# Performance work log

Hardware: AMD Instinct MI355X
Metric: run time of the kernel (lower is better)

Reference implementation:

```python
import jax, jax.numpy as jnp
import numpy as np

E, D, A, F, K = 512, 1024, 128, 32, 31  # encoder_dim, decoder_dim, attention_dim, location_filters, kernel
B, T = 128, 512


def setup_inputs() -> dict:
    key = jax.random.key(0)
    ks = jax.random.split(key, 9)
    s = lambda *sh: 1.0 / np.sqrt(sh[-1])
    return {
        "encoder_outputs": jax.random.normal(ks[0], (B, T, E), jnp.float32),
        "decoder_state": jax.random.normal(ks[1], (B, D), jnp.float32),
        "prev_attention_weights": jax.random.uniform(ks[2], (B, T), jnp.float32),
        # parameters (torch Linear stores [out, in]; Conv1d [out, in, K])
        "W_enc": jax.random.normal(ks[3], (A, E), jnp.float32) * s(A, E),
        "W_dec": jax.random.normal(ks[4], (A, D), jnp.float32) * s(A, D),
        "conv_w": jax.random.normal(ks[5], (F, 1, K), jnp.float32) * (1.0 / np.sqrt(K)),
        "W_loc": jax.random.normal(ks[6], (A, F), jnp.float32) * s(A, F),
        "W_e": jax.random.normal(ks[7], (1, A), jnp.float32) * s(1, A),
        "b_e": jax.random.normal(ks[8], (1,), jnp.float32) * 0.01,
    }


def reference(encoder_outputs, decoder_state, prev_attention_weights,
              W_enc, W_dec, conv_w, W_loc, W_e, b_e):
    # encoder projection: [B,T,E] @ [E,A] -> [B,T,A]
    enc_p = jnp.einsum('bte,ae->bta', encoder_outputs, W_enc)
    # decoder projection: [B,D] -> [B,1,A]
    dec_p = jnp.einsum('bd,ad->ba', decoder_state, W_dec)[:, None, :]
    # location conv: [B,1,T] * [F,1,K] -> [B,F,T], 'same' padding
    loc = jax.lax.conv_general_dilated(
        prev_attention_weights[:, None, :], conv_w,
        window_strides=(1,), padding=[((K - 1) // 2, (K - 1) // 2)],
        dimension_numbers=('NCH', 'OIH', 'NCH'))
    # [B,F,T] -> [B,T,A]
    loc_p = jnp.einsum('bft,af->bta', loc, W_loc)
    # energies: [B,T]
    energies = jnp.einsum('bta,a->bt', jnp.tanh(enc_p + dec_p + loc_p), W_e[0]) + b_e[0]
    attention_weights = jax.nn.softmax(energies, axis=1)
    # context: [B,T] x [B,T,E] -> [B,E]
    context_vector = jnp.einsum('bt,bte->be', attention_weights, encoder_outputs)
    return context_vector, attention_weights
```

## Files before the change

kernel.cpp:

```cpp
#include <hip/hip_runtime.h>
#include <hip/hip_bf16.h>
#include <math.h>

namespace {
constexpr int EDIM  = 512;
constexpr int DDIM  = 1024;
constexpr int ADIM  = 128;
constexpr int FDIM  = 32;
constexpr int KW    = 31;
constexpr int BATCH = 128;
constexpr int TDIM  = 512;

constexpr int LSTR = 40;
constexpr int TILE = 128 * LSTR;

typedef __attribute__((ext_vector_type(8))) short short8;
typedef __attribute__((ext_vector_type(4))) float floatx4;

__device__ __forceinline__ float fast_tanh(float x) {
  x = fminf(9.0f, fmaxf(-9.0f, x));
  float e = __expf(2.0f * x);
  return (e - 1.0f) / (e + 1.0f);
}

__device__ __forceinline__ ushort2 pack_bf16(float x, float y) {
  union { __hip_bfloat162 h; ushort2 u; } cv;
  cv.h = __float22bfloat162_rn(make_float2(x, y));
  return cv.u;
}

__device__ __forceinline__ short8 pack8(floatx4 a, floatx4 b) {
  union { ushort2 u[4]; short8 v; } o;
  o.u[0] = pack_bf16(a[0], a[1]); o.u[1] = pack_bf16(a[2], a[3]);
  o.u[2] = pack_bf16(b[0], b[1]); o.u[3] = pack_bf16(b[2], b[3]);
  return o.v;
}

__device__ __forceinline__ int ld_acq(int* p) {
  return __hip_atomic_load(p, __ATOMIC_ACQUIRE, __HIP_MEMORY_SCOPE_WORKGROUP);
}
__device__ __forceinline__ void add_rel(int* p) {
  __hip_atomic_fetch_add(p, 1, __ATOMIC_RELEASE, __HIP_MEMORY_SCOPE_WORKGROUP);
}

__global__ __launch_bounds__(256)
void dec_proj_kernel(const float* __restrict__ dec,
                     const float* __restrict__ Wdec,
                     float* __restrict__ dec_p) {
  int b = blockIdx.x, az = blockIdx.y;
  int tid = threadIdx.x;
  int al = tid >> 3, seg = tid & 7;
  int a = az * 32 + al;
  const float* dv = dec + (size_t)b * DDIM;
  const float* wv = Wdec + (size_t)a * DDIM;
  float s = 0.f;
  #pragma unroll 8
  for (int it = 0; it < 32; ++it) {
    int d = it * 32 + seg * 4;
    float4 d4 = *(const float4*)(dv + d);
    float4 w4 = *(const float4*)(wv + d);
    s += d4.x * w4.x + d4.y * w4.y + d4.z * w4.z + d4.w * w4.w;
  }
  s += __shfl_xor(s, 1, 64);
  s += __shfl_xor(s, 2, 64);
  s += __shfl_xor(s, 4, 64);
  if (seg == 0) dec_p[b * ADIM + a] = s;
}

__global__ __launch_bounds__(768)
void energies_kernel(const float* __restrict__ enc,
                     const float* __restrict__ Wenc,
                     const float* __restrict__ pa,
                     const float* __restrict__ convw,
                     const float* __restrict__ Wloc,
                     const float* __restrict__ We,
                     const float* __restrict__ be,
                     const float* __restrict__ dec_p,
                     float* __restrict__ energ) {
  __shared__ ushort tiles[2 * 2 * TILE];
  __shared__ ushort convS[4096];
  __shared__ float pa_s[160];
  __shared__ float cw_t[KW * 32];
  __shared__ int ready_a[2], ready_b[2], done_c[2], conv_done;

  const int tid  = threadIdx.x;
  const int b    = blockIdx.y;
  const int t0b  = blockIdx.x * 128;
  const int wave = tid >> 6, lane = tid & 63;

  if (tid == 0) {
    ready_a[0] = ready_a[1] = ready_b[0] = ready_b[1] = 0;
    done_c[0] = done_c[1] = 0;
    conv_done = 0;
  }
  if (tid >= 512 && tid < 512 + 158) {
    int gt = t0b - 15 + (tid - 512);
    pa_s[tid - 512] = (gt >= 0 && gt < TDIM) ? pa[b * TDIM + gt] : 0.f;
  }
  if (tid < 512)
    for (int id = tid; id < FDIM * KW; id += 512)
      cw_t[(id % KW) * 32 + (id / KW)] = convw[id];
  __syncthreads();

  if (wave >= 8) {
    const bool isA = (wave < 10);
    const int p = wave & 1;
    const float* gbase = isA ? enc + ((size_t)(b * TDIM + t0b)) * EDIM : Wenc;
    ushort* lbase = tiles + (isA ? 0 : TILE);
    int* myready = isA ? ready_a : ready_b;

    floatx4 v[8];
    #pragma unroll
    for (int j = 0; j < 4; ++j) {
      int idx = j * 64 + lane;
      int row = p * 64 + (idx >> 2), c = idx & 3;
      const float* g = gbase + (size_t)row * EDIM + c * 8;
      v[2 * j]     = *(const floatx4*)g;
      v[2 * j + 1] = *(const floatx4*)(g + 4);
    }

    for (int kt = 0; kt < 16; ++kt) {
      const int s = kt & 1, i = kt >> 1;
      if (kt >= 2)
        while (ld_acq(&done_c[s]) < 8 * i) __builtin_amdgcn_s_sleep(10);
      ushort* slot = lbase + s * 2 * TILE;
      #pragma unroll
      for (int j = 0; j < 4; ++j) {
        int idx = j * 64 + lane;
        int row = p * 64 + (idx >> 2), c = idx & 3;
        *(short8*)&slot[row * LSTR + c * 8] = pack8(v[2 * j], v[2 * j + 1]);
      }
      __threadfence_block();
      if (lane == 0) add_rel(&myready[s]);
      if (kt < 15) {
        #pragma unroll
        for (int j = 0; j < 4; ++j) {
          int idx = j * 64 + lane;
          int row = p * 64 + (idx >> 2), c = idx & 3;
          const float* g = gbase + (size_t)row * EDIM + (kt + 1) * 32 + c * 8;
          v[2 * j]     = *(const floatx4*)g;
          v[2 * j + 1] = *(const floatx4*)(g + 4);
        }
      }
    }
    return;
  }

  const int lc = lane & 15, lq = lane >> 4;

  {
    const int tl = tid >> 2, fg = tid & 3;
    float cv[8] = {0.f, 0.f, 0.f, 0.f, 0.f, 0.f, 0.f, 0.f};
    #pragma unroll
    for (int k = 0; k < KW; ++k) {
      float p = pa_s[tl + k];
      floatx4 c0 = *(const floatx4*)&cw_t[k * 32 + fg * 8];
      floatx4 c1 = *(const floatx4*)&cw_t[k * 32 + fg * 8 + 4];
      #pragma unroll
      for (int n = 0; n < 4; ++n) cv[n] += p * c0[n];
      #pragma unroll
      for (int n = 0; n < 4; ++n) cv[4 + n] += p * c1[n];
    }
    *(short8*)&convS[tl * 32 + fg * 8] =
        pack8((floatx4){cv[0], cv[1], cv[2], cv[3]},
              (floatx4){cv[4], cv[5], cv[6], cv[7]});
  }
  __threadfence_block();
  if (lane == 0) add_rel(&conv_done);

  floatx4 acc[8];
  #pragma unroll
  for (int aT = 0; aT < 8; ++aT) acc[aT] = (floatx4){0.f, 0.f, 0.f, 0.f};

  for (int kt = 0; kt < 16; ++kt) {
    const int s = kt & 1, i = kt >> 1;
    const int need = 2 * (i + 1);
    while (ld_acq(&ready_a[s]) < need || ld_acq(&ready_b[s]) < need)
      __builtin_amdgcn_s_sleep(6);
    const ushort* As_ = tiles + s * 2 * TILE;
    const ushort* Bs_ = As_ + TILE;
    short8 af = *(const short8*)&As_[(wave * 16 + lc) * LSTR + lq * 8];
    #pragma unroll
    for (int aT = 0; aT < 8; ++aT) {
      short8 bf = *(const short8*)&Bs_[(aT * 16 + lc) * LSTR + lq * 8];
      acc[aT] = __builtin_amdgcn_mfma_f32_16x16x32_bf16(af, bf, acc[aT], 0, 0, 0);
    }
    if (lane == 0) add_rel(&done_c[s]);
  }

  while (ld_acq(&conv_done) < 8) __builtin_amdgcn_s_sleep(6);
  {
    short8 afl = *(const short8*)&convS[(wave * 16 + lc) * 32 + lq * 8];
    #pragma unroll
    for (int aT = 0; aT < 8; ++aT) {
      const float* g = Wloc + (size_t)(aT * 16 + lc) * FDIM + lq * 8;
      short8 bfl = pack8(*(const floatx4*)g, *(const floatx4*)(g + 4));
      acc[aT] = __builtin_amdgcn_mfma_f32_16x16x32_bf16(afl, bfl, acc[aT], 0, 0, 0);
    }
  }

  const float be0 = be[0];
  float dpv[8], wev[8];
  #pragma unroll
  for (int aT = 0; aT < 8; ++aT) {
    int a = aT * 16 + lc;
    dpv[aT] = dec_p[b * ADIM + a];
    wev[aT] = We[a];
  }
  {
    float es[4] = {0.f, 0.f, 0.f, 0.f};
    #pragma unroll
    for (int aT = 0; aT < 8; ++aT)
      #pragma unroll
      for (int i = 0; i < 4; ++i)
        es[i] += fast_tanh(acc[aT][i] + dpv[aT]) * wev[aT];
    #pragma unroll
    for (int m = 1; m < 16; m <<= 1)
      #pragma unroll
      for (int i = 0; i < 4; ++i) es[i] += __shfl_xor(es[i], m, 64);
    if (lc == 0) {
      floatx4 ev = {es[0] + be0, es[1] + be0, es[2] + be0, es[3] + be0};
      *(floatx4*)&energ[(size_t)b * TDIM + t0b + wave * 16 + lq * 4] = ev;
    }
  }
}

__global__ __launch_bounds__(256)
void softmax_context_kernel(const float* __restrict__ enc,
                            const float* __restrict__ energ,
                            float* __restrict__ attn,
                            float* __restrict__ ctx) {
  __shared__ float aw[TDIM];
  __shared__ float redm[4];
  __shared__ float reds[4];
  __shared__ float red2[8][128];
  const int b = blockIdx.y, ex = blockIdx.x, tid = threadIdx.x;
  const float* row = energ + (size_t)b * TDIM;
  float x0 = row[tid], x1 = row[tid + 256];
  float m = fmaxf(x0, x1);
  #pragma unroll
  for (int off = 32; off; off >>= 1) m = fmaxf(m, __shfl_xor(m, off, 64));
  int wid = tid >> 6, lane = tid & 63;
  if (lane == 0) redm[wid] = m;
  __syncthreads();
  m = fmaxf(fmaxf(redm[0], redm[1]), fmaxf(redm[2], redm[3]));
  float e0 = __expf(x0 - m), e1 = __expf(x1 - m);
  float s = e0 + e1;
  #pragma unroll
  for (int off = 32; off; off >>= 1) s += __shfl_xor(s, off, 64);
  if (lane == 0) reds[wid] = s;
  __syncthreads();
  s = reds[0] + reds[1] + reds[2] + reds[3];
  float inv = 1.0f / s;
  float w0 = e0 * inv, w1 = e1 * inv;
  aw[tid] = w0; aw[tid + 256] = w1;
  if (ex == 0) {
    attn[(size_t)b * TDIM + tid] = w0;
    attn[(size_t)b * TDIM + tid + 256] = w1;
  }
  __syncthreads();
  const int c4 = (tid & 31) * 4;
  const int h  = tid >> 5;
  const float* ep = enc + (size_t)b * TDIM * EDIM + ex * 128 + c4;
  float4 acc = make_float4(0.f, 0.f, 0.f, 0.f);
  #pragma unroll 16
  for (int t = h; t < TDIM; t += 8) {
    float w = aw[t];
    float4 v = *(const float4*)(ep + (size_t)t * EDIM);
    acc.x += w * v.x; acc.y += w * v.y; acc.z += w * v.z; acc.w += w * v.w;
  }
  *(float4*)&red2[h][c4] = acc;
  __syncthreads();
  if (tid < 128) {
    float sum = 0.f;
    #pragma unroll
    for (int g = 0; g < 8; ++g) sum += red2[g][tid];
    ctx[(size_t)b * EDIM + ex * 128 + tid] = sum;
  }
}

__global__ __launch_bounds__(256)
void softmax_context_inplace_kernel(const float* __restrict__ enc,
                                    float* __restrict__ attn,
                                    float* __restrict__ ctx) {
  __shared__ float aw[TDIM];
  __shared__ float redm[4];
  __shared__ float reds[4];
  const int b = blockIdx.y, tid = threadIdx.x;
  float* row = attn + (size_t)b * TDIM;
  float x0 = row[tid], x1 = row[tid + 256];
  float m = fmaxf(x0, x1);
  #pragma unroll
  for (int off = 32; off; off >>= 1) m = fmaxf(m, __shfl_xor(m, off, 64));
  int wid = tid >> 6, lane = tid & 63;
  if (lane == 0) redm[wid] = m;
  __syncthreads();
  m = fmaxf(fmaxf(redm[0], redm[1]), fmaxf(redm[2], redm[3]));
  float e0 = __expf(x0 - m), e1 = __expf(x1 - m);
  float s = e0 + e1;
  #pragma unroll
  for (int off = 32; off; off >>= 1) s += __shfl_xor(s, off, 64);
  if (lane == 0) reds[wid] = s;
  __syncthreads();
  s = reds[0] + reds[1] + reds[2] + reds[3];
  float inv = 1.0f / s;
  float w0 = e0 * inv, w1 = e1 * inv;
  row[tid] = w0; row[tid + 256] = w1;
  aw[tid] = w0; aw[tid + 256] = w1;
  __syncthreads();
  const float* ep = enc + ((size_t)b * TDIM) * EDIM;
  float a0 = 0.f, a1 = 0.f;
  #pragma unroll 8
  for (int t = 0; t < TDIM; ++t) {
    float w = aw[t];
    a0 += w * ep[(size_t)t * EDIM + tid];
    a1 += w * ep[(size_t)t * EDIM + tid + 256];
  }
  ctx[(size_t)b * EDIM + tid] = a0;
  ctx[(size_t)b * EDIM + tid + 256] = a1;
}

}

extern "C" void kernel_launch(void* const* d_in, const int* in_sizes, int n_in,
                              void* d_out, int out_size, void* d_ws, size_t ws_size,
                              hipStream_t stream) {
  const float* enc   = (const float*)d_in[0];
  const float* dec   = (const float*)d_in[1];
  const float* pa    = (const float*)d_in[2];
  const float* Wenc  = (const float*)d_in[3];
  const float* Wdec  = (const float*)d_in[4];
  const float* convw = (const float*)d_in[5];
  const float* Wloc  = (const float*)d_in[6];
  const float* We    = (const float*)d_in[7];
  const float* be    = (const float*)d_in[8];

  float* ctx  = (float*)d_out;
  float* attn = (float*)d_out + BATCH * EDIM;

  float* dec_p = (float*)d_ws;
  float* energ = dec_p + BATCH * ADIM;

  const size_t need = (size_t)(BATCH * ADIM + BATCH * TDIM) * sizeof(float);

  dim3 g1(BATCH, 4);
  dec_proj_kernel<<<g1, 256, 0, stream>>>(dec, Wdec, dec_p);

  dim3 g2(TDIM / 128, BATCH);
  if (ws_size >= need) {
    energies_kernel<<<g2, 768, 0, stream>>>(enc, Wenc, pa, convw, Wloc, We, be,
                                            dec_p, energ);
    dim3 g3(4, BATCH);
    softmax_context_kernel<<<g3, 256, 0, stream>>>(enc, energ, attn, ctx);
  } else {
    energies_kernel<<<g2, 768, 0, stream>>>(enc, Wenc, pa, convw, Wloc, We, be,
                                            dec_p, attn);
    dim3 g3(1, BATCH);
    softmax_context_inplace_kernel<<<g3, 256, 0, stream>>>(enc, attn, ctx);
  }
}
```

Before: 243.4 us.

## Fuse softmax and context into energies kernel with split-softmax last-block reduction

Each energies block now computes a local max and sum over its 128 time steps, forms unnormalized weights, and accumulates a partial context from the encoder tile it just covered. It writes those partials to the workspace. The last block per batch, found through an atomic counter reset in dec_proj, rescales and combines them into the final attention weights and context. This removes the separate softmax/context launch and its second full pass over encoder_outputs from global memory. The cost is extra shared memory, atomics and a serialized tail in the last block of each batch.

```diff
diff --git a/kernel.cpp b/kernel.cpp
--- a/kernel.cpp
+++ b/kernel.cpp
@@ -46,9 +46,11 @@
 __global__ __launch_bounds__(256)
 void dec_proj_kernel(const float* __restrict__ dec,
                      const float* __restrict__ Wdec,
-                     float* __restrict__ dec_p) {
+                     float* __restrict__ dec_p,
+                     int* __restrict__ counters) {
   int b = blockIdx.x, az = blockIdx.y;
   int tid = threadIdx.x;
+  if (counters && az == 0 && tid == 0) counters[b] = 0;
   int al = tid >> 3, seg = tid & 7;
   int a = az * 32 + al;
   const float* dv = dec + (size_t)b * DDIM;
@@ -67,6 +69,7 @@
   if (seg == 0) dec_p[b * ADIM + a] = s;
 }
 
+template <int FUSED>
 __global__ __launch_bounds__(768)
 void energies_kernel(const float* __restrict__ enc,
                      const float* __restrict__ Wenc,
@@ -76,16 +79,29 @@
                      const float* __restrict__ We,
                      const float* __restrict__ be,
                      const float* __restrict__ dec_p,
-                     float* __restrict__ energ) {
+                     float* __restrict__ energ,
+                     float* __restrict__ pm,
+                     float* __restrict__ ps,
+                     float* __restrict__ pctx,
+                     int*   __restrict__ counters,
+                     float* __restrict__ attn,
+                     float* __restrict__ ctx) {
   __shared__ ushort tiles[2 * 2 * TILE];
   __shared__ ushort convS[4096];
   __shared__ float pa_s[160];
   __shared__ float cw_t[KW * 32];
   __shared__ int ready_a[2], ready_b[2], done_c[2], conv_done;
+  __shared__ float e_s[128];
+  __shared__ float aw_s[128];
+  __shared__ float ms[2];
+  __shared__ float red2[6][512];
+  __shared__ float pmx[4], psx[4];
+  __shared__ int lastflag;
 
   const int tid  = threadIdx.x;
   const int b    = blockIdx.y;
-  const int t0b  = blockIdx.x * 128;
+  const int chunk = blockIdx.x;
+  const int t0b  = chunk * 128;
   const int wave = tid >> 6, lane = tid & 63;
 
   if (tid == 0) {
@@ -143,139 +159,150 @@
         }
       }
     }
-    return;
-  }
-
-  const int lc = lane & 15, lq = lane >> 4;
+  } else {
+    const int lc = lane & 15, lq = lane >> 4;
+
+    {
+      const int tl = tid >> 2, fg = tid & 3;
+      float cv[8] = {0.f, 0.f, 0.f, 0.f, 0.f, 0.f, 0.f, 0.f};
+      #pragma unroll
+      for (int k = 0; k < KW; ++k) {
+        float p = pa_s[tl + k];
+        floatx4 c0 = *(const floatx4*)&cw_t[k * 32 + fg * 8];
+        floatx4 c1 = *(const floatx4*)&cw_t[k * 32 + fg * 8 + 4];
+        #pragma unroll
+        for (int n = 0; n < 4; ++n) cv[n] += p * c0[n];
+        #pragma unroll
+        for (int n = 0; n < 4; ++n) cv[4 + n] += p * c1[n];
+      }
+      *(short8*)&convS[tl * 32 + fg * 8] =
+          pack8((floatx4){cv[0], cv[1], cv[2], cv[3]},
+                (floatx4){cv[4], cv[5], cv[6], cv[7]});
+    }
+    __threadfence_block();
+    if (lane == 0) add_rel(&conv_done);
+
+    floatx4 acc[8];
+    #pragma unroll
+    for (int aT = 0; aT < 8; ++aT) acc[aT] = (floatx4){0.f, 0.f, 0.f, 0.f};
+
+    for (int kt = 0; kt < 16; ++kt) {
+      const int s = kt & 1, i = kt >> 1;
+      const int need = 2 * (i + 1);
+      while (ld_acq(&ready_a[s]) < need || ld_acq(&ready_b[s]) < need)
+        __builtin_amdgcn_s_sleep(6);
+      const ushort* As_ = tiles + s * 2 * TILE;
+      const ushort* Bs_ = As_ + TILE;
+      short8 af = *(const short8*)&As_[(wave * 16 + lc) * LSTR + lq * 8];
+      #pragma unroll
+      for (int aT = 0; aT < 8; ++aT) {
+        short8 bf = *(const short8*)&Bs_[(aT * 16 + lc) * LSTR + lq * 8];
+        acc[aT] = __builtin_amdgcn_mfma_f32_16x16x32_bf16(af, bf, acc[aT], 0, 0, 0);
+      }
+      if (lane == 0) add_rel(&done_c[s]);
+    }
+
+    while (ld_acq(&conv_done) < 8) __builtin_amdgcn_s_sleep(6);
+    {
+      short8 afl = *(const short8*)&convS[(wave * 16 + lc) * 32 + lq * 8];
+      #pragma unroll
+      for (int aT = 0; aT < 8; ++aT) {
+        const float* g = Wloc + (size_t)(aT * 16 + lc) * FDIM + lq * 8;
+        short8 bfl = pack8(*(const floatx4*)g, *(const floatx4*)(g + 4));
+        acc[aT] = __builtin_amdgcn_mfma_f32_16x16x32_bf16(afl, bfl, acc[aT], 0, 0, 0);
+      }
+    }
+
+    const float be0 = be[0];
+    float dpv[8], wev[8];
+    #pragma unroll
+    for (int aT = 0; aT < 8; ++aT) {
+      int a = aT * 16 + lc;
+      dpv[aT] = dec_p[b * ADIM + a];
+      wev[aT] = We[a];
+    }
+    {
+      float es[4] = {0.f, 0.f, 0.f, 0.f};
+      #pragma unroll
+      for (int aT = 0; aT < 8; ++aT)
+        #pragma unroll
+        for (int i = 0; i < 4; ++i)
+          es[i] += fast_tanh(acc[aT][i] + dpv[aT]) * wev[aT];
+      #pragma unroll
+      for (int m = 1; m < 16; m <<= 1)
+        #pragma unroll
+        for (int i = 0; i < 4; ++i) es[i] += __shfl_xor(es[i], m, 64);
+      if (lc == 0) {
+        floatx4 ev = {es[0] + be0, es[1] + be0, es[2] + be0, es[3] + be0};
+        *(floatx4*)&energ[(size_t)b * TDIM + t0b + wave * 16 + lq * 4] = ev;
+        if (FUSED) *(floatx4*)&e_s[wave * 16 + lq * 4] = ev;
+      }
+    }
+  }
+
+  if constexpr (!FUSED) return;
+
+  __syncthreads();
+
+  if (wave == 0) {
+    float x0 = e_s[lane], x1 = e_s[lane + 64];
+    float m = fmaxf(x0, x1);
+    #pragma unroll
+    for (int off = 1; off < 64; off <<= 1) m = fmaxf(m, __shfl_xor(m, off, 64));
+    float sum = __expf(x0 - m) + __expf(x1 - m);
+    #pragma unroll
+    for (int off = 1; off < 64; off <<= 1) sum += __shfl_xor(sum, off, 64);
+    if (lane == 0) {
+      ms[0] = m;
+      pm[b * 4 + chunk] = m;
+      ps[b * 4 + chunk] = sum;
+    }
+  }
+  __syncthreads();
+  const float mI = ms[0];
+  if (tid < 128) aw_s[tid] = __expf(e_s[tid] - mI);
+  __syncthreads();
 
   {
-    const int tl = tid >> 2, fg = tid & 3;
-    float cv[8] = {0.f, 0.f, 0.f, 0.f, 0.f, 0.f, 0.f, 0.f};
-    #pragma unroll
-    for (int k = 0; k < KW; ++k) {
-      float p = pa_s[tl + k];
-      floatx4 c0 = *(const floatx4*)&cw_t[k * 32 + fg * 8];
-      floatx4 c1 = *(const floatx4*)&cw_t[k * 32 + fg * 8 + 4];
-      #pragma unroll
-      for (int n = 0; n < 4; ++n) cv[n] += p * c0[n];
-      #pragma unroll
-      for (int n = 0; n < 4; ++n) cv[4 + n] += p * c1[n];
-    }
-    *(short8*)&convS[tl * 32 + fg * 8] =
-        pack8((floatx4){cv[0], cv[1], cv[2], cv[3]},
-              (floatx4){cv[4], cv[5], cv[6], cv[7]});
-  }
-  __threadfence_block();
-  if (lane == 0) add_rel(&conv_done);
-
-  floatx4 acc[8];
-  #pragma unroll
-  for (int aT = 0; aT < 8; ++aT) acc[aT] = (floatx4){0.f, 0.f, 0.f, 0.f};
-
-  for (int kt = 0; kt < 16; ++kt) {
-    const int s = kt & 1, i = kt >> 1;
-    const int need = 2 * (i + 1);
-    while (ld_acq(&ready_a[s]) < need || ld_acq(&ready_b[s]) < need)
-      __builtin_amdgcn_s_sleep(6);
-    const ushort* As_ = tiles + s * 2 * TILE;
-    const ushort* Bs_ = As_ + TILE;
-    short8 af = *(const short8*)&As_[(wave * 16 + lc) * LSTR + lq * 8];
-    #pragma unroll
-    for (int aT = 0; aT < 8; ++aT) {
-      short8 bf = *(const short8*)&Bs_[(aT * 16 + lc) * LSTR + lq * 8];
-      acc[aT] = __builtin_amdgcn_mfma_f32_16x16x32_bf16(af, bf, acc[aT], 0, 0, 0);
-    }
-    if (lane == 0) add_rel(&done_c[s]);
-  }
-
-  while (ld_acq(&conv_done) < 8) __builtin_amdgcn_s_sleep(6);
-  {
-    short8 afl = *(const short8*)&convS[(wave * 16 + lc) * 32 + lq * 8];
-    #pragma unroll
-    for (int aT = 0; aT < 8; ++aT) {
-      const float* g = Wloc + (size_t)(aT * 16 + lc) * FDIM + lq * 8;
-      short8 bfl = pack8(*(const floatx4*)g, *(const floatx4*)(g + 4));
-      acc[aT] = __builtin_amdgcn_mfma_f32_16x16x32_bf16(afl, bfl, acc[aT], 0, 0, 0);
-    }
-  }
-
-  const float be0 = be[0];
-  float dpv[8], wev[8];
-  #pragma unroll
-  for (int aT = 0; aT < 8; ++aT) {
-    int a = aT * 16 + lc;
-    dpv[aT] = dec_p[b * ADIM + a];
-    wev[aT] = We[a];
-  }
-  {
-    float es[4] = {0.f, 0.f, 0.f, 0.f};
-    #pragma unroll
-    for (int aT = 0; aT < 8; ++aT)
-      #pragma unroll
-      for (int i = 0; i < 4; ++i)
-        es[i] += fast_tanh(acc[aT][i] + dpv[aT]) * wev[aT];
-    #pragma unroll
-    for (int m = 1; m < 16; m <<= 1)
-      #pragma unroll
-      for (int i = 0; i < 4; ++i) es[i] += __shfl_xor(es[i], m, 64);
-    if (lc == 0) {
-      floatx4 ev = {es[0] + be0, es[1] + be0, es[2] + be0, es[3] + be0};
-      *(floatx4*)&energ[(size_t)b * TDIM + t0b + wave * 16 + lq * 4] = ev;
-    }
-  }
-}
-
-__global__ __launch_bounds__(256)
-void softmax_context_kernel(const float* __restrict__ enc,
-                            const float* __restrict__ energ,
-                            float* __restrict__ attn,
-                            float* __restrict__ ctx) {
-  __shared__ float aw[TDIM];
-  __shared__ float redm[4];
-  __shared__ float reds[4];
-  __shared__ float red2[8][128];
-  const int b = blockIdx.y, ex = blockIdx.x, tid = threadIdx.x;
-  const float* row = energ + (size_t)b * TDIM;
-  float x0 = row[tid], x1 = row[tid + 256];
-  float m = fmaxf(x0, x1);
-  #pragma unroll
-  for (int off = 32; off; off >>= 1) m = fmaxf(m, __shfl_xor(m, off, 64));
-  int wid = tid >> 6, lane = tid & 63;
-  if (lane == 0) redm[wid] = m;
-  __syncthreads();
-  m = fmaxf(fmaxf(redm[0], redm[1]), fmaxf(redm[2], redm[3]));
-  float e0 = __expf(x0 - m), e1 = __expf(x1 - m);
-  float s = e0 + e1;
-  #pragma unroll
-  for (int off = 32; off; off >>= 1) s += __shfl_xor(s, off, 64);
-  if (lane == 0) reds[wid] = s;
-  __syncthreads();
-  s = reds[0] + reds[1] + reds[2] + reds[3];
-  float inv = 1.0f / s;
-  float w0 = e0 * inv, w1 = e1 * inv;
-  aw[tid] = w0; aw[tid + 256] = w1;
-  if (ex == 0) {
-    attn[(size_t)b * TDIM + tid] = w0;
-    attn[(size_t)b * TDIM + tid + 256] = w1;
-  }
-  __syncthreads();
-  const int c4 = (tid & 31) * 4;
-  const int h  = tid >> 5;
-  const float* ep = enc + (size_t)b * TDIM * EDIM + ex * 128 + c4;
-  float4 acc = make_float4(0.f, 0.f, 0.f, 0.f);
-  #pragma unroll 16
-  for (int t = h; t < TDIM; t += 8) {
-    float w = aw[t];
-    float4 v = *(const float4*)(ep + (size_t)t * EDIM);
-    acc.x += w * v.x; acc.y += w * v.y; acc.z += w * v.z; acc.w += w * v.w;
-  }
-  *(float4*)&red2[h][c4] = acc;
-  __syncthreads();
-  if (tid < 128) {
-    float sum = 0.f;
-    #pragma unroll
-    for (int g = 0; g < 8; ++g) sum += red2[g][tid];
-    ctx[(size_t)b * EDIM + ex * 128 + tid] = sum;
+    const int tg = tid >> 7;
+    const int c4 = (tid & 127) * 4;
+    const float* ep = enc + ((size_t)(b * TDIM + t0b)) * EDIM + c4;
+    float4 acc = make_float4(0.f, 0.f, 0.f, 0.f);
+    for (int t = tg; t < 128; t += 6) {
+      float w = aw_s[t];
+      float4 v = *(const float4*)(ep + (size_t)t * EDIM);
+      acc.x += w * v.x; acc.y += w * v.y; acc.z += w * v.z; acc.w += w * v.w;
+    }
+    *(float4*)&red2[tg][c4] = acc;
+  }
+  __syncthreads();
+  if (tid < 512) {
+    float v = 0.f;
+    #pragma unroll
+    for (int g = 0; g < 6; ++g) v += red2[g][tid];
+    pctx[((size_t)(b * 4 + chunk)) * EDIM + tid] = v;
+  }
+  __threadfence();
+  __syncthreads();
+  if (tid == 0)
+    lastflag = __hip_atomic_fetch_add(&counters[b], 1, __ATOMIC_ACQ_REL,
+                                      __HIP_MEMORY_SCOPE_AGENT);
+  __syncthreads();
+  if (lastflag != 3) return;
+
+  if (tid < 4) { pmx[tid] = pm[b * 4 + tid]; psx[tid] = ps[b * 4 + tid]; }
+  __syncthreads();
+  const float M = fmaxf(fmaxf(pmx[0], pmx[1]), fmaxf(pmx[2], pmx[3]));
+  float r0 = __expf(pmx[0] - M), r1 = __expf(pmx[1] - M);
+  float r2 = __expf(pmx[2] - M), r3 = __expf(pmx[3] - M);
+  const float S = psx[0] * r0 + psx[1] * r1 + psx[2] * r2 + psx[3] * r3;
+  const float inv = 1.0f / S;
+  if (tid < 512) {
+    float e = energ[(size_t)b * TDIM + tid];
+    attn[(size_t)b * TDIM + tid] = __expf(e - M) * inv;
+    const float* pc = pctx + (size_t)b * 4 * EDIM + tid;
+    float c = pc[0] * r0 + pc[EDIM] * r1 + pc[2 * EDIM] * r2 + pc[3 * EDIM] * r3;
+    ctx[(size_t)b * EDIM + tid] = c * inv;
   }
 }
 
@@ -340,21 +367,28 @@
 
   float* dec_p = (float*)d_ws;
   float* energ = dec_p + BATCH * ADIM;
-
-  const size_t need = (size_t)(BATCH * ADIM + BATCH * TDIM) * sizeof(float);
-
-  dim3 g1(BATCH, 4);
-  dec_proj_kernel<<<g1, 256, 0, stream>>>(dec, Wdec, dec_p);
+  float* pm    = energ + BATCH * TDIM;
+  float* ps    = pm + BATCH * 4;
+  float* pctx  = ps + BATCH * 4;
+  int*   cnts  = (int*)(pctx + (size_t)BATCH * 4 * EDIM);
+
+  const size_t need =
+      ((size_t)BATCH * ADIM + BATCH * TDIM + BATCH * 8 +
+       (size_t)BATCH * 4 * EDIM) * sizeof(float) + BATCH * sizeof(int);
 
   dim3 g2(TDIM / 128, BATCH);
   if (ws_size >= need) {
-    energies_kernel<<<g2, 768, 0, stream>>>(enc, Wenc, pa, convw, Wloc, We, be,
-                                            dec_p, energ);
-    dim3 g3(4, BATCH);
-    softmax_context_kernel<<<g3, 256, 0, stream>>>(enc, energ, attn, ctx);
+    dim3 g1(BATCH, 4);
+    dec_proj_kernel<<<g1, 256, 0, stream>>>(dec, Wdec, dec_p, cnts);
+    energies_kernel<1><<<g2, 768, 0, stream>>>(enc, Wenc, pa, convw, Wloc, We,
+                                               be, dec_p, energ, pm, ps, pctx,
+                                               cnts, attn, ctx);
   } else {
-    energies_kernel<<<g2, 768, 0, stream>>>(enc, Wenc, pa, convw, Wloc, We, be,
-                                            dec_p, attn);
+    dim3 g1(BATCH, 4);
+    dec_proj_kernel<<<g1, 256, 0, stream>>>(dec, Wdec, dec_p, nullptr);
+    energies_kernel<0><<<g2, 768, 0, stream>>>(enc, Wenc, pa, convw, Wloc, We,
+                                               be, dec_p, attn, nullptr, nullptr,
+                                               nullptr, nullptr, nullptr, nullptr);
     dim3 g3(1, BATCH);
     softmax_context_inplace_kernel<<<g3, 256, 0, stream>>>(enc, attn, ctx);
   }
```

Measured after the change: 409.8 us. +68.3%, slower.

## Replace producer/consumer warp specialization with uniform double-buffered loads and barriers

Applied to the files above, without the earlier changes.

The energies kernel previously used four dedicated producer waves that loaded encoder and weight tiles into shared memory and signalled consumer waves through workgroup-scope atomic flags with sleep-polling. Now all eight waves load their own slice of the next K-tile into registers, compute MFMAs on the current buffer, then store the next tile, with one __syncthreads per iteration. The conv result reuses the A buffer after the loop instead of its own array. This removes spin-wait polling and the extra waves, and cuts shared memory, at the cost of losing dedicated producer overlap and adding block-wide barriers.

```diff
diff --git a/kernel.cpp b/kernel.cpp
--- a/kernel.cpp
+++ b/kernel.cpp
@@ -12,7 +12,6 @@
 constexpr int TDIM  = 512;
 
 constexpr int LSTR = 40;
-constexpr int TILE = 128 * LSTR;
 
 typedef __attribute__((ext_vector_type(8))) short short8;
 typedef __attribute__((ext_vector_type(4))) float floatx4;
@@ -34,13 +33,6 @@
   o.u[0] = pack_bf16(a[0], a[1]); o.u[1] = pack_bf16(a[2], a[3]);
   o.u[2] = pack_bf16(b[0], b[1]); o.u[3] = pack_bf16(b[2], b[3]);
   return o.v;
-}
-
-__device__ __forceinline__ int ld_acq(int* p) {
-  return __hip_atomic_load(p, __ATOMIC_ACQUIRE, __HIP_MEMORY_SCOPE_WORKGROUP);
-}
-__device__ __forceinline__ void add_rel(int* p) {
-  __hip_atomic_fetch_add(p, 1, __ATOMIC_RELEASE, __HIP_MEMORY_SCOPE_WORKGROUP);
 }
 
 __global__ __launch_bounds__(256)
@@ -67,7 +59,7 @@
   if (seg == 0) dec_p[b * ADIM + a] = s;
 }
 
-__global__ __launch_bounds__(768)
+__global__ __launch_bounds__(512)
 void energies_kernel(const float* __restrict__ enc,
                      const float* __restrict__ Wenc,
                      const float* __restrict__ pa,
@@ -77,80 +69,37 @@
                      const float* __restrict__ be,
                      const float* __restrict__ dec_p,
                      float* __restrict__ energ) {
-  __shared__ ushort tiles[2 * 2 * TILE];
-  __shared__ ushort convS[4096];
+  __shared__ ushort A_s[2][128 * LSTR];
+  __shared__ ushort B_s[2][128 * LSTR];
+  __shared__ float cw_t[KW * 32];
   __shared__ float pa_s[160];
-  __shared__ float cw_t[KW * 32];
-  __shared__ int ready_a[2], ready_b[2], done_c[2], conv_done;
 
   const int tid  = threadIdx.x;
   const int b    = blockIdx.y;
   const int t0b  = blockIdx.x * 128;
   const int wave = tid >> 6, lane = tid & 63;
-
-  if (tid == 0) {
-    ready_a[0] = ready_a[1] = ready_b[0] = ready_b[1] = 0;
-    done_c[0] = done_c[1] = 0;
-    conv_done = 0;
-  }
-  if (tid >= 512 && tid < 512 + 158) {
-    int gt = t0b - 15 + (tid - 512);
-    pa_s[tid - 512] = (gt >= 0 && gt < TDIM) ? pa[b * TDIM + gt] : 0.f;
-  }
-  if (tid < 512)
-    for (int id = tid; id < FDIM * KW; id += 512)
-      cw_t[(id % KW) * 32 + (id / KW)] = convw[id];
-  __syncthreads();
-
-  if (wave >= 8) {
-    const bool isA = (wave < 10);
-    const int p = wave & 1;
-    const float* gbase = isA ? enc + ((size_t)(b * TDIM + t0b)) * EDIM : Wenc;
-    ushort* lbase = tiles + (isA ? 0 : TILE);
-    int* myready = isA ? ready_a : ready_b;
-
-    floatx4 v[8];
-    #pragma unroll
-    for (int j = 0; j < 4; ++j) {
-      int idx = j * 64 + lane;
-      int row = p * 64 + (idx >> 2), c = idx & 3;
-      const float* g = gbase + (size_t)row * EDIM + c * 8;
-      v[2 * j]     = *(const floatx4*)g;
-      v[2 * j + 1] = *(const floatx4*)(g + 4);
-    }
-
-    for (int kt = 0; kt < 16; ++kt) {
-      const int s = kt & 1, i = kt >> 1;
-      if (kt >= 2)
-        while (ld_acq(&done_c[s]) < 8 * i) __builtin_amdgcn_s_sleep(10);
-      ushort* slot = lbase + s * 2 * TILE;
-      #pragma unroll
-      for (int j = 0; j < 4; ++j) {
-        int idx = j * 64 + lane;
-        int row = p * 64 + (idx >> 2), c = idx & 3;
-        *(short8*)&slot[row * LSTR + c * 8] = pack8(v[2 * j], v[2 * j + 1]);
-      }
-      __threadfence_block();
-      if (lane == 0) add_rel(&myready[s]);
-      if (kt < 15) {
-        #pragma unroll
-        for (int j = 0; j < 4; ++j) {
-          int idx = j * 64 + lane;
-          int row = p * 64 + (idx >> 2), c = idx & 3;
-          const float* g = gbase + (size_t)row * EDIM + (kt + 1) * 32 + c * 8;
-          v[2 * j]     = *(const floatx4*)g;
-          v[2 * j + 1] = *(const floatx4*)(g + 4);
-        }
-      }
-    }
-    return;
-  }
-
   const int lc = lane & 15, lq = lane >> 4;
 
+  if (tid < 158) {
+    int gt = t0b - 15 + tid;
+    pa_s[tid] = (gt >= 0 && gt < TDIM) ? pa[b * TDIM + gt] : 0.f;
+  }
+  for (int id = tid; id < FDIM * KW; id += 512)
+    cw_t[(id % KW) * 32 + (id / KW)] = convw[id];
+  __syncthreads();
+
+  const int srow = tid >> 2, scs = tid & 3;
+  const float* aBase =
+      enc + ((size_t)(b * TDIM + t0b) + srow) * EDIM + scs * 8;
+  const float* bBase = Wenc + (size_t)srow * EDIM + scs * 8;
+  const int sdst = srow * LSTR + scs * 8;
+
+  floatx4 la0 = *(const floatx4*)aBase, la1 = *(const floatx4*)(aBase + 4);
+  floatx4 lb0 = *(const floatx4*)bBase, lb1 = *(const floatx4*)(bBase + 4);
+
+  float cv[8] = {0.f, 0.f, 0.f, 0.f, 0.f, 0.f, 0.f, 0.f};
   {
     const int tl = tid >> 2, fg = tid & 3;
-    float cv[8] = {0.f, 0.f, 0.f, 0.f, 0.f, 0.f, 0.f, 0.f};
     #pragma unroll
     for (int k = 0; k < KW; ++k) {
       float p = pa_s[tl + k];
@@ -161,36 +110,49 @@
       #pragma unroll
       for (int n = 0; n < 4; ++n) cv[4 + n] += p * c1[n];
     }
-    *(short8*)&convS[tl * 32 + fg * 8] =
-        pack8((floatx4){cv[0], cv[1], cv[2], cv[3]},
-              (floatx4){cv[4], cv[5], cv[6], cv[7]});
-  }
-  __threadfence_block();
-  if (lane == 0) add_rel(&conv_done);
+  }
+
+  *(short8*)&A_s[0][sdst] = pack8(la0, la1);
+  *(short8*)&B_s[0][sdst] = pack8(lb0, lb1);
 
   floatx4 acc[8];
   #pragma unroll
   for (int aT = 0; aT < 8; ++aT) acc[aT] = (floatx4){0.f, 0.f, 0.f, 0.f};
 
   for (int kt = 0; kt < 16; ++kt) {
-    const int s = kt & 1, i = kt >> 1;
-    const int need = 2 * (i + 1);
-    while (ld_acq(&ready_a[s]) < need || ld_acq(&ready_b[s]) < need)
-      __builtin_amdgcn_s_sleep(6);
-    const ushort* As_ = tiles + s * 2 * TILE;
-    const ushort* Bs_ = As_ + TILE;
+    __syncthreads();
+    if (kt < 15) {
+      la0 = *(const floatx4*)(aBase + (kt + 1) * 32);
+      la1 = *(const floatx4*)(aBase + (kt + 1) * 32 + 4);
+      lb0 = *(const floatx4*)(bBase + (kt + 1) * 32);
+      lb1 = *(const floatx4*)(bBase + (kt + 1) * 32 + 4);
+    }
+    const ushort* As_ = A_s[kt & 1];
+    const ushort* Bs_ = B_s[kt & 1];
     short8 af = *(const short8*)&As_[(wave * 16 + lc) * LSTR + lq * 8];
     #pragma unroll
     for (int aT = 0; aT < 8; ++aT) {
       short8 bf = *(const short8*)&Bs_[(aT * 16 + lc) * LSTR + lq * 8];
       acc[aT] = __builtin_amdgcn_mfma_f32_16x16x32_bf16(af, bf, acc[aT], 0, 0, 0);
     }
-    if (lane == 0) add_rel(&done_c[s]);
-  }
-
-  while (ld_acq(&conv_done) < 8) __builtin_amdgcn_s_sleep(6);
+    if (kt < 15) {
+      const int d = (kt + 1) & 1;
+      *(short8*)&A_s[d][sdst] = pack8(la0, la1);
+      *(short8*)&B_s[d][sdst] = pack8(lb0, lb1);
+    }
+  }
+  __syncthreads();
+
   {
-    short8 afl = *(const short8*)&convS[(wave * 16 + lc) * 32 + lq * 8];
+    const int tl = tid >> 2, fg = tid & 3;
+    *(short8*)&A_s[0][tl * LSTR + fg * 8] =
+        pack8((floatx4){cv[0], cv[1], cv[2], cv[3]},
+              (floatx4){cv[4], cv[5], cv[6], cv[7]});
+  }
+  __syncthreads();
+
+  {
+    short8 afl = *(const short8*)&A_s[0][(wave * 16 + lc) * LSTR + lq * 8];
     #pragma unroll
     for (int aT = 0; aT < 8; ++aT) {
       const float* g = Wloc + (size_t)(aT * 16 + lc) * FDIM + lq * 8;
@@ -348,12 +310,12 @@
 
   dim3 g2(TDIM / 128, BATCH);
   if (ws_size >= need) {
-    energies_kernel<<<g2, 768, 0, stream>>>(enc, Wenc, pa, convw, Wloc, We, be,
+    energies_kernel<<<g2, 512, 0, stream>>>(enc, Wenc, pa, convw, Wloc, We, be,
                                             dec_p, energ);
     dim3 g3(4, BATCH);
     softmax_context_kernel<<<g3, 256, 0, stream>>>(enc, energ, attn, ctx);
   } else {
-    energies_kernel<<<g2, 768, 0, stream>>>(enc, Wenc, pa, convw, Wloc, We, be,
+    energies_kernel<<<g2, 512, 0, stream>>>(enc, Wenc, pa, convw, Wloc, We, be,
                                             dec_p, attn);
     dim3 g3(1, BATCH);
     softmax_context_inplace_kernel<<<g3, 256, 0, stream>>>(enc, attn, ctx);
```

After: 278.9 us. 14.6% more time.

## Split context reduction over time chunks with partial sums and combine kernel

Applied to the files above, without the earlier changes.

Adds a split-T variant of the softmax/context stage: each block handles one 128-column E slice and one 128-step T chunk, writing partial context sums to workspace, and a small combine kernel adds the four partials. This raises the grid from 512 to 2048 blocks so the bandwidth-bound pass over encoder outputs gets more parallelism and latency hiding. The cost is an extra kernel launch, a partial-sum buffer round trip, and every block recomputing the full softmax max and sum. The path runs only when the workspace is large enough.

```diff
diff --git a/kernel.cpp b/kernel.cpp
--- a/kernel.cpp
+++ b/kernel.cpp
@@ -226,6 +226,71 @@
 }
 
 __global__ __launch_bounds__(256)
+void softmax_context_part_kernel(const float* __restrict__ enc,
+                                 const float* __restrict__ energ,
+                                 float* __restrict__ attn,
+                                 float* __restrict__ pctx) {
+  __shared__ float aw[128];
+  __shared__ float redm[4];
+  __shared__ float reds[4];
+  __shared__ float red2[8][128];
+  const int b = blockIdx.y, tid = threadIdx.x;
+  const int ex = blockIdx.x & 3, tc = blockIdx.x >> 2;
+  const float* row = energ + (size_t)b * TDIM;
+  float x0 = row[tid], x1 = row[tid + 256];
+  float m = fmaxf(x0, x1);
+  #pragma unroll
+  for (int off = 32; off; off >>= 1) m = fmaxf(m, __shfl_xor(m, off, 64));
+  int wid = tid >> 6, lane = tid & 63;
+  if (lane == 0) redm[wid] = m;
+  __syncthreads();
+  m = fmaxf(fmaxf(redm[0], redm[1]), fmaxf(redm[2], redm[3]));
+  float e0 = __expf(x0 - m), e1 = __expf(x1 - m);
+  float s = e0 + e1;
+  #pragma unroll
+  for (int off = 32; off; off >>= 1) s += __shfl_xor(s, off, 64);
+  if (lane == 0) reds[wid] = s;
+  __syncthreads();
+  s = reds[0] + reds[1] + reds[2] + reds[3];
+  const float inv = 1.0f / s;
+  if (tid < 128) {
+    float w = __expf(row[tc * 128 + tid] - m) * inv;
+    aw[tid] = w;
+    if (ex == 0) attn[(size_t)b * TDIM + tc * 128 + tid] = w;
+  }
+  __syncthreads();
+  const int c4 = (tid & 31) * 4;
+  const int h  = tid >> 5;
+  const float* ep =
+      enc + ((size_t)(b * TDIM + tc * 128)) * EDIM + ex * 128 + c4;
+  float4 acc = make_float4(0.f, 0.f, 0.f, 0.f);
+  #pragma unroll
+  for (int t = h; t < 128; t += 8) {
+    float w = aw[t];
+    float4 v = *(const float4*)(ep + (size_t)t * EDIM);
+    acc.x += w * v.x; acc.y += w * v.y; acc.z += w * v.z; acc.w += w * v.w;
+  }
+  *(float4*)&red2[h][c4] = acc;
+  __syncthreads();
+  if (tid < 128) {
+    float sum = 0.f;
+    #pragma unroll
+    for (int g = 0; g < 8; ++g) sum += red2[g][tid];
+    pctx[((size_t)tc * BATCH + b) * EDIM + ex * 128 + tid] = sum;
+  }
+}
+
+__global__ __launch_bounds__(512)
+void combine_ctx_kernel(const float* __restrict__ pctx,
+                        float* __restrict__ ctx) {
+  const int b = blockIdx.x, e = threadIdx.x;
+  const size_t off = (size_t)b * EDIM + e;
+  const size_t st  = (size_t)BATCH * EDIM;
+  ctx[off] = pctx[off] + pctx[off + st] + pctx[off + 2 * st] +
+             pctx[off + 3 * st];
+}
+
+__global__ __launch_bounds__(256)
 void softmax_context_kernel(const float* __restrict__ enc,
                             const float* __restrict__ energ,
                             float* __restrict__ attn,
@@ -340,14 +405,25 @@
 
   float* dec_p = (float*)d_ws;
   float* energ = dec_p + BATCH * ADIM;
-
-  const size_t need = (size_t)(BATCH * ADIM + BATCH * TDIM) * sizeof(float);
+  float* pctx  = energ + BATCH * TDIM;
+
+  const size_t need_split =
+      ((size_t)BATCH * ADIM + BATCH * TDIM + 4 * (size_t)BATCH * EDIM) *
+      sizeof(float);
+  const size_t need_r1 =
+      (size_t)(BATCH * ADIM + BATCH * TDIM) * sizeof(float);
 
   dim3 g1(BATCH, 4);
   dec_proj_kernel<<<g1, 256, 0, stream>>>(dec, Wdec, dec_p);
 
   dim3 g2(TDIM / 128, BATCH);
-  if (ws_size >= need) {
+  if (ws_size >= need_split) {
+    energies_kernel<<<g2, 768, 0, stream>>>(enc, Wenc, pa, convw, Wloc, We, be,
+                                            dec_p, energ);
+    dim3 g3(16, BATCH);
+    softmax_context_part_kernel<<<g3, 256, 0, stream>>>(enc, energ, attn, pctx);
+    combine_ctx_kernel<<<dim3(BATCH), 512, 0, stream>>>(pctx, ctx);
+  } else if (ws_size >= need_r1) {
     energies_kernel<<<g2, 768, 0, stream>>>(enc, Wenc, pa, convw, Wloc, We, be,
                                             dec_p, energ);
     dim3 g3(4, BATCH);
```

New measurement: 245.3 us. No clear change (+0.8%).
